# Kernel tuning notes

Measured on AMD Instinct MI355X. Metric: run time of the kernel, lower is better.

The kernel has to match this reference:

```python
import jax, jax.numpy as jnp
import numpy as np

N = 40000   # nodes
E = 600000  # edges
F = 128     # feature/hidden dim
G = 64      # graphs in batch


def setup_inputs() -> dict:
    key = jax.random.key(0)
    ks = jax.random.split(key, 16)
    x = jax.random.normal(ks[0], (N, F), dtype=jnp.float32)
    src = jax.random.randint(ks[1], (E,), 0, N)
    dst = jax.random.randint(ks[2], (E,), 0, N)
    edge_index = jnp.stack([src, dst]).astype(jnp.int64)
    batch = jnp.sort(jax.random.randint(ks[3], (N,), 0, G)).astype(jnp.int64)
    s = 1.0 / np.sqrt(F)
    W0 = jax.random.normal(ks[4], (F, F), dtype=jnp.float32) * s
    b0 = jnp.zeros((F,), dtype=jnp.float32)
    W1 = jax.random.normal(ks[5], (F, F), dtype=jnp.float32) * s
    b1 = jnp.zeros((F,), dtype=jnp.float32)
    W2 = jax.random.normal(ks[6], (F, F), dtype=jnp.float32) * s
    b2 = jnp.zeros((F,), dtype=jnp.float32)
    lin_w = jax.random.normal(ks[7], (F, 1), dtype=jnp.float32) * s
    lin_b = jnp.zeros((1,), dtype=jnp.float32)
    return {"x": x, "edge_index": edge_index, "batch": batch,
            "W0": W0, "b0": b0, "W1": W1, "b1": b1, "W2": W2, "b2": b2,
            "lin_w": lin_w, "lin_b": lin_b}


def _gcn_conv(x, W, b, src, dst, norm, num_nodes):
    # PyG GCNConv: linear transform, gather source, normalize, scatter-add to dst, add bias
    h = x @ W                                  # [N, F_out]
    msg = h[src] * norm[:, None]               # [E+N, F_out]
    agg = jax.ops.segment_sum(msg, dst, num_segments=num_nodes)
    return agg + b


def reference(x, edge_index, batch, W0, b0, W1, b1, W2, b2, lin_w, lin_b):
    num_nodes = x.shape[0]
    loops = jnp.arange(num_nodes, dtype=edge_index.dtype)
    src = jnp.concatenate([edge_index[0], loops])   # add self-loops
    dst = jnp.concatenate([edge_index[1], loops])
    # symmetric normalization deg^-1/2 (degree over in-edges incl. self loops)
    deg = jax.ops.segment_sum(jnp.ones_like(src, dtype=x.dtype), dst,
                              num_segments=num_nodes)
    dinv = jnp.where(deg > 0, jax.lax.rsqrt(jnp.maximum(deg, 1e-12)), 0.0)
    norm = dinv[src] * dinv[dst]                    # [E+N]

    h = jax.nn.relu(_gcn_conv(x, W0, b0, src, dst, norm, num_nodes))
    h = jax.nn.relu(_gcn_conv(h, W1, b1, src, dst, norm, num_nodes))
    h = jax.nn.relu(_gcn_conv(h, W2, b2, src, dst, norm, num_nodes))

    # global_mean_pool over ragged graph segments
    sums = jax.ops.segment_sum(h, batch, num_segments=G)            # [G, F]
    counts = jax.ops.segment_sum(jnp.ones((num_nodes,), h.dtype), batch,
                                 num_segments=G)                    # [G]
    pooled = sums / jnp.maximum(counts, 1.0)[:, None]
    return pooled @ lin_w + lin_b                                   # [G, 1]
```

## Files before the change

### kernel.cpp

```cpp
#include <hip/hip_runtime.h>
#include <hip/hip_bf16.h>

#define F_DIM 128
#define POOL_SEG 16

typedef __attribute__((ext_vector_type(8))) short short8v;
typedef __attribute__((ext_vector_type(4))) float float4v;


__device__ __forceinline__ ushort f2bf(float f) {
    uint u = __float_as_uint(f);
    u += 0x7fffu + ((u >> 16) & 1u);
    return (ushort)(u >> 16);
}
__device__ __forceinline__ float bf2f(ushort h) {
    return __uint_as_float(((uint)h) << 16);
}
__device__ __forceinline__ void bf2x(uint u, float& a, float& b) {
    a = __uint_as_float((u & 0x0000ffffu) << 16);
    b = __uint_as_float(u & 0xffff0000u);
}


__global__ void count_kernel(const int* __restrict__ dst, int* __restrict__ deg, int E_) {
    int i = blockIdx.x * blockDim.x + threadIdx.x;
    if (i < E_) atomicAdd(&deg[dst[i]], 1);
}

__global__ void scan_blocksums_kernel(const int* __restrict__ deg, int* __restrict__ bsum, int N_) {
    __shared__ int s[256];
    int i = blockIdx.x * 256 + threadIdx.x;
    s[threadIdx.x] = (i < N_) ? deg[i] : 0;
    __syncthreads();
    for (int off = 128; off; off >>= 1) {
        if (threadIdx.x < off) s[threadIdx.x] += s[threadIdx.x + off];
        __syncthreads();
    }
    if (threadIdx.x == 0) bsum[blockIdx.x] = s[0];
}

__global__ void scan_bs_kernel(const int* __restrict__ bsum, int* __restrict__ bsx, int NB) {
    __shared__ int s[256];
    int t = threadIdx.x;
    int orig = (t < NB) ? bsum[t] : 0;
    s[t] = orig;
    __syncthreads();
    for (int off = 1; off < 256; off <<= 1) {
        int v = (t >= off) ? s[t - off] : 0;
        __syncthreads();
        s[t] += v;
        __syncthreads();
    }
    if (t < NB) bsx[t] = s[t] - orig;
}

__global__ void scan_final_kernel(const int* __restrict__ deg, const int* __restrict__ bsx,
                                  int* __restrict__ row_ptr, int* __restrict__ rfill,
                                  float* __restrict__ dinv, int N_, int E_) {
    __shared__ int s[256];
    int t = threadIdx.x;
    int i = blockIdx.x * 256 + t;
    int orig = (i < N_) ? deg[i] : 0;
    s[t] = orig;
    __syncthreads();
    for (int off = 1; off < 256; off <<= 1) {
        int v = (t >= off) ? s[t - off] : 0;
        __syncthreads();
        s[t] += v;
        __syncthreads();
    }
    int excl = s[t] - orig + bsx[blockIdx.x];
    if (i < N_) {
        row_ptr[i] = excl;
        rfill[i] = excl;
        dinv[i] = 1.0f / sqrtf((float)(orig + 1));
    }
    if (i == N_ - 1) row_ptr[N_] = E_;
}

__global__ void fill_kernel(const int* __restrict__ src, const int* __restrict__ dst,
                            int* __restrict__ cur, int* __restrict__ col_src, int E_) {
    int i = blockIdx.x * blockDim.x + threadIdx.x;
    if (i < E_) {
        int p = atomicAdd(&cur[dst[i]], 1);
        col_src[p] = src[i];
    }
}


__global__ __launch_bounds__(256) void wprep_kernel(
    const float* __restrict__ W0, const float* __restrict__ W1, const float* __restrict__ W2,
    ushort* __restrict__ Wth, ushort* __restrict__ Wtl)
{
    int layer = blockIdx.x >> 4;
    int chunkc = blockIdx.x & 15;
    const float* W = (layer == 0) ? W0 : (layer == 1) ? W1 : W2;
    int t = threadIdx.x;
    int c  = chunkc * 8 + (t >> 5);
    int k0 = (t & 31) * 4;
    ushort4 hi, lo;
    float v0 = W[(size_t)(k0 + 0) * F_DIM + c];
    float v1 = W[(size_t)(k0 + 1) * F_DIM + c];
    float v2 = W[(size_t)(k0 + 2) * F_DIM + c];
    float v3 = W[(size_t)(k0 + 3) * F_DIM + c];
    hi.x = f2bf(v0); lo.x = f2bf(v0 - bf2f(hi.x));
    hi.y = f2bf(v1); lo.y = f2bf(v1 - bf2f(hi.y));
    hi.z = f2bf(v2); lo.z = f2bf(v2 - bf2f(hi.z));
    hi.w = f2bf(v3); lo.w = f2bf(v3 - bf2f(hi.w));
    size_t o = (size_t)layer * F_DIM * F_DIM + (size_t)c * F_DIM + k0;
    *reinterpret_cast<ushort4*>(&Wth[o]) = hi;
    *reinterpret_cast<ushort4*>(&Wtl[o]) = lo;
}


__global__ __launch_bounds__(256) void gemm_scale_kernel(
    const float* __restrict__ in, const ushort* __restrict__ Wth, const ushort* __restrict__ Wtl,
    const float* __restrict__ dinv, ushort* __restrict__ outbf, int N_)
{
    __shared__ ushort Ah[64 * F_DIM];
    __shared__ ushort Al[64 * F_DIM];
    __shared__ ushort Bh[64 * F_DIM];
    __shared__ ushort Bl[64 * F_DIM];

    const int tid = threadIdx.x;
    const int brow = (blockIdx.x >> 1) * 64;
    const int bcol = (blockIdx.x & 1) * 64;

    #pragma unroll
    for (int i = 0; i < 4; ++i) {
        int chunk = tid + i * 256;
        int r  = chunk >> 4;
        int k0 = (chunk & 15) * 8;
        int row = brow + r;
        float f[8];
        if (row < N_) {
            float4 g0 = *reinterpret_cast<const float4*>(&in[(size_t)row * F_DIM + k0]);
            float4 g1 = *reinterpret_cast<const float4*>(&in[(size_t)row * F_DIM + k0 + 4]);
            f[0] = g0.x; f[1] = g0.y; f[2] = g0.z; f[3] = g0.w;
            f[4] = g1.x; f[5] = g1.y; f[6] = g1.z; f[7] = g1.w;
        } else {
            #pragma unroll
            for (int j = 0; j < 8; ++j) f[j] = 0.f;
        }
        ushort hi[8], lo[8];
        #pragma unroll
        for (int j = 0; j < 8; ++j) {
            hi[j] = f2bf(f[j]);
            lo[j] = f2bf(f[j] - bf2f(hi[j]));
        }
        int idx = r * F_DIM + (k0 ^ ((r & 7) << 3));
        *reinterpret_cast<short8v*>(&Ah[idx]) = *reinterpret_cast<short8v*>(hi);
        *reinterpret_cast<short8v*>(&Al[idx]) = *reinterpret_cast<short8v*>(lo);
    }
    #pragma unroll
    for (int i = 0; i < 4; ++i) {
        int chunk = tid + i * 256;
        int c  = chunk >> 4;
        int k0 = (chunk & 15) * 8;
        size_t go = (size_t)(bcol + c) * F_DIM + k0;
        int idx = c * F_DIM + (k0 ^ ((c & 7) << 3));
        *reinterpret_cast<short8v*>(&Bh[idx]) = *reinterpret_cast<const short8v*>(&Wth[go]);
        *reinterpret_cast<short8v*>(&Bl[idx]) = *reinterpret_cast<const short8v*>(&Wtl[go]);
    }
    __syncthreads();

    const int l = tid & 63;
    const int wave = tid >> 6;
    const int m0 = wave * 16;
    const int row_a = m0 + (l & 15);
    const int kgrp = (l >> 4) * 8;
    const int aswz = (row_a & 7) << 3;

    float4v acc[4] = {{0.f,0.f,0.f,0.f},{0.f,0.f,0.f,0.f},{0.f,0.f,0.f,0.f},{0.f,0.f,0.f,0.f}};

    #pragma unroll
    for (int kk = 0; kk < 4; ++kk) {
        int kbase = kk * 32 + kgrp;
        short8v a_h = *reinterpret_cast<short8v*>(&Ah[row_a * F_DIM + (kbase ^ aswz)]);
        short8v a_l = *reinterpret_cast<short8v*>(&Al[row_a * F_DIM + (kbase ^ aswz)]);
        #pragma unroll
        for (int n = 0; n < 4; ++n) {
            int col_b = n * 16 + (l & 15);
            int bidx = col_b * F_DIM + (kbase ^ ((col_b & 7) << 3));
            short8v b_h = *reinterpret_cast<short8v*>(&Bh[bidx]);
            short8v b_l = *reinterpret_cast<short8v*>(&Bl[bidx]);
            acc[n] = __builtin_amdgcn_mfma_f32_16x16x32_bf16(a_h, b_h, acc[n], 0, 0, 0);
            acc[n] = __builtin_amdgcn_mfma_f32_16x16x32_bf16(a_l, b_h, acc[n], 0, 0, 0);
            acc[n] = __builtin_amdgcn_mfma_f32_16x16x32_bf16(a_h, b_l, acc[n], 0, 0, 0);
        }
    }

    #pragma unroll
    for (int i = 0; i < 4; ++i) {
        int rloc = m0 + (l >> 4) * 4 + i;
        int row = brow + rloc;
        if (row < N_) {
            float s = dinv[row];
            #pragma unroll
            for (int n = 0; n < 4; ++n) {
                ushort o = f2bf(s * acc[n][i]);
                outbf[(size_t)row * F_DIM + bcol + n * 16 + (l & 15)] = o;
            }
        }
    }
}


__global__ __launch_bounds__(256) void gather_kernel(
    const ushort* __restrict__ Mbf, const int* __restrict__ row_ptr,
    const int* __restrict__ col_src, const float* __restrict__ dinv,
    const float* __restrict__ bias, float* __restrict__ Hout, int N_)
{
    int v = blockIdx.x * 4 + (threadIdx.x >> 6);
    if (v >= N_) return;
    const int lane = threadIdx.x & 63;
    const int fq  = lane & 15;
    const int sub = lane >> 4;
    const uint4* M4 = reinterpret_cast<const uint4*>(Mbf);

    float acc[8];
    if (sub == 0) {
        uint4 u = M4[(size_t)v * 16 + fq];
        bf2x(u.x, acc[0], acc[1]);
        bf2x(u.y, acc[2], acc[3]);
        bf2x(u.z, acc[4], acc[5]);
        bf2x(u.w, acc[6], acc[7]);
    } else {
        #pragma unroll
        for (int j = 0; j < 8; ++j) acc[j] = 0.f;
    }

    int lo = row_ptr[v], hi = row_ptr[v + 1];
    int e = lo;
    for (; e + 12 <= hi; e += 12) {
        int s0 = col_src[e + sub];
        int s1 = col_src[e + 4 + sub];
        int s2 = col_src[e + 8 + sub];
        uint4 u0 = M4[(size_t)s0 * 16 + fq];
        uint4 u1 = M4[(size_t)s1 * 16 + fq];
        uint4 u2 = M4[(size_t)s2 * 16 + fq];
        float a, b;
        bf2x(u0.x, a, b); acc[0] += a; acc[1] += b;
        bf2x(u0.y, a, b); acc[2] += a; acc[3] += b;
        bf2x(u0.z, a, b); acc[4] += a; acc[5] += b;
        bf2x(u0.w, a, b); acc[6] += a; acc[7] += b;
        bf2x(u1.x, a, b); acc[0] += a; acc[1] += b;
        bf2x(u1.y, a, b); acc[2] += a; acc[3] += b;
        bf2x(u1.z, a, b); acc[4] += a; acc[5] += b;
        bf2x(u1.w, a, b); acc[6] += a; acc[7] += b;
        bf2x(u2.x, a, b); acc[0] += a; acc[1] += b;
        bf2x(u2.y, a, b); acc[2] += a; acc[3] += b;
        bf2x(u2.z, a, b); acc[4] += a; acc[5] += b;
        bf2x(u2.w, a, b); acc[6] += a; acc[7] += b;
    }
    for (; e + 4 <= hi; e += 4) {
        int s = col_src[e + sub];
        uint4 u = M4[(size_t)s * 16 + fq];
        float a, b;
        bf2x(u.x, a, b); acc[0] += a; acc[1] += b;
        bf2x(u.y, a, b); acc[2] += a; acc[3] += b;
        bf2x(u.z, a, b); acc[4] += a; acc[5] += b;
        bf2x(u.w, a, b); acc[6] += a; acc[7] += b;
    }
    if (e + sub < hi) {
        int s = col_src[e + sub];
        uint4 u = M4[(size_t)s * 16 + fq];
        float a, b;
        bf2x(u.x, a, b); acc[0] += a; acc[1] += b;
        bf2x(u.y, a, b); acc[2] += a; acc[3] += b;
        bf2x(u.z, a, b); acc[4] += a; acc[5] += b;
        bf2x(u.w, a, b); acc[6] += a; acc[7] += b;
    }

    #pragma unroll
    for (int j = 0; j < 8; ++j) {
        acc[j] += __shfl_xor(acc[j], 16);
        acc[j] += __shfl_xor(acc[j], 32);
    }

    if (sub == 0) {
        float dv = dinv[v];
        const float4* b4 = reinterpret_cast<const float4*>(bias);
        float4 bb0 = b4[fq * 2], bb1 = b4[fq * 2 + 1];
        float4 o0, o1;
        o0.x = fmaxf(dv * acc[0] + bb0.x, 0.0f);
        o0.y = fmaxf(dv * acc[1] + bb0.y, 0.0f);
        o0.z = fmaxf(dv * acc[2] + bb0.z, 0.0f);
        o0.w = fmaxf(dv * acc[3] + bb0.w, 0.0f);
        o1.x = fmaxf(dv * acc[4] + bb1.x, 0.0f);
        o1.y = fmaxf(dv * acc[5] + bb1.y, 0.0f);
        o1.z = fmaxf(dv * acc[6] + bb1.z, 0.0f);
        o1.w = fmaxf(dv * acc[7] + bb1.w, 0.0f);
        float4* H4 = reinterpret_cast<float4*>(&Hout[(size_t)v * F_DIM + fq * 8]);
        H4[0] = o0;
        H4[1] = o1;
    }
}


__device__ __forceinline__ int lower_bound_i(const int* __restrict__ a, int n, int key) {
    int lo = 0, hi = n;
    while (lo < hi) {
        int mid = (lo + hi) >> 1;
        if (a[mid] < key) lo = mid + 1; else hi = mid;
    }
    return lo;
}

__global__ __launch_bounds__(128) void pool_part_kernel(
    const float* __restrict__ H, const int* __restrict__ batch,
    float* __restrict__ partial, int N_)
{
    int g = blockIdx.x / POOL_SEG;
    int s = blockIdx.x % POOL_SEG;
    int lo = lower_bound_i(batch, N_, g);
    int hi = lower_bound_i(batch, N_, g + 1);
    int len = hi - lo;
    int chunk = (len + POOL_SEG - 1) / POOL_SEG;
    int a = lo + s * chunk;
    int b = min(a + chunk, hi);
    int col = threadIdx.x;
    float acc = 0.f;
    for (int n = a; n < b; ++n) acc += H[(size_t)n * F_DIM + col];
    partial[((size_t)g * POOL_SEG + s) * F_DIM + col] = acc;
}

__global__ __launch_bounds__(128) void pool_final_kernel(
    const float* __restrict__ partial, const int* __restrict__ batch,
    const float* __restrict__ lin_w, const float* __restrict__ lin_b,
    float* __restrict__ out, int N_)
{
    int g = blockIdx.x;
    int col = threadIdx.x;
    float acc = 0.f;
    #pragma unroll
    for (int s = 0; s < POOL_SEG; ++s)
        acc += partial[((size_t)g * POOL_SEG + s) * F_DIM + col];
    int lo = lower_bound_i(batch, N_, g);
    int hi = lower_bound_i(batch, N_, g + 1);
    float pooled = acc / fmaxf((float)(hi - lo), 1.0f);
    float v = pooled * lin_w[col];
    __shared__ float sm[128];
    sm[col] = v;
    __syncthreads();
    if (col < 64) {
        float t = sm[col] + sm[col + 64];
        for (int off = 32; off; off >>= 1) t += __shfl_down(t, off);
        if (col == 0) out[g] = t + lin_b[0];
    }
}


extern "C" void kernel_launch(void* const* d_in, const int* in_sizes, int n_in,
                              void* d_out, int out_size, void* d_ws, size_t ws_size,
                              hipStream_t stream) {
    const float* x     = (const float*)d_in[0];
    const int*   ei    = (const int*)d_in[1];
    const int*   batch = (const int*)d_in[2];
    const float* W0    = (const float*)d_in[3];
    const float* b0    = (const float*)d_in[4];
    const float* W1    = (const float*)d_in[5];
    const float* b1    = (const float*)d_in[6];
    const float* W2    = (const float*)d_in[7];
    const float* b2    = (const float*)d_in[8];
    const float* lin_w = (const float*)d_in[9];
    const float* lin_b = (const float*)d_in[10];

    const int N_ = in_sizes[2];
    const int E_ = in_sizes[1] / 2;
    const int G_ = out_size;
    const int* esrc = ei;
    const int* edst = ei + E_;

    char* p = reinterpret_cast<char*>(d_ws);
    ushort* Mbf = reinterpret_cast<ushort*>(p);        p += (size_t)N_ * F_DIM * sizeof(ushort);
    float*  Hbuf = reinterpret_cast<float*>(p);        p += (size_t)N_ * F_DIM * sizeof(float);
    float*  dinvp = reinterpret_cast<float*>(p);       p += (size_t)N_ * sizeof(float);
    int*    deg = reinterpret_cast<int*>(p);           p += (size_t)N_ * sizeof(int);
    int*    row_ptr = reinterpret_cast<int*>(p);       p += (size_t)(N_ + 4) * sizeof(int);
    int*    rfill = reinterpret_cast<int*>(p);         p += (size_t)N_ * sizeof(int);
    int*    col_src = reinterpret_cast<int*>(p);       p += (size_t)E_ * sizeof(int);
    ushort* Wth = reinterpret_cast<ushort*>(p);        p += (size_t)3 * F_DIM * F_DIM * sizeof(ushort);
    ushort* Wtl = reinterpret_cast<ushort*>(p);        p += (size_t)3 * F_DIM * F_DIM * sizeof(ushort);
    const int NB = (N_ + 255) / 256;
    int*    bsum = reinterpret_cast<int*>(p);          p += (size_t)NB * sizeof(int);
    int*    bsx = reinterpret_cast<int*>(p);
    float*  partial = reinterpret_cast<float*>(d_ws);

    hipMemsetAsync(deg, 0, (size_t)N_ * sizeof(int), stream);

    int eb = (E_ + 255) / 256;
    wprep_kernel<<<48, 256, 0, stream>>>(W0, W1, W2, Wth, Wtl);
    count_kernel<<<eb, 256, 0, stream>>>(edst, deg, E_);
    scan_blocksums_kernel<<<NB, 256, 0, stream>>>(deg, bsum, N_);
    scan_bs_kernel<<<1, 256, 0, stream>>>(bsum, bsx, NB);
    scan_final_kernel<<<NB, 256, 0, stream>>>(deg, bsx, row_ptr, rfill, dinvp, N_, E_);
    fill_kernel<<<eb, 256, 0, stream>>>(esrc, edst, rfill, col_src, E_);

    const int gemm_grid = ((N_ + 63) / 64) * 2;
    const int gat_grid  = (N_ + 3) / 4;

    const float* cur_in = x;
    const float* bias[3] = {b0, b1, b2};
    for (int l = 0; l < 3; ++l) {
        gemm_scale_kernel<<<gemm_grid, 256, 0, stream>>>(
            cur_in, Wth + (size_t)l * F_DIM * F_DIM, Wtl + (size_t)l * F_DIM * F_DIM,
            dinvp, Mbf, N_);
        gather_kernel<<<gat_grid, 256, 0, stream>>>(
            Mbf, row_ptr, col_src, dinvp, bias[l], Hbuf, N_);
        cur_in = Hbuf;
    }

    pool_part_kernel<<<G_ * POOL_SEG, 128, 0, stream>>>(Hbuf, batch, partial, N_);
    pool_final_kernel<<<G_, 128, 0, stream>>>(partial, batch, lin_w, lin_b, (float*)d_out, N_);
}
```

Measured before the change: 228.2 us.

## Cooperatively load neighbor indices per wave and fold deg zeroing into prep kernel

The gather kernel now loads up to 64 neighbor indices at once, one per lane, with the self-loop treated as the first entry. Lanes then broadcast indices with shuffles and issue four row loads per iteration, and a masked tail handles the remainder. This replaces per-subgroup scalar col_src loads and the separate self-row load, aiming for more memory-level parallelism and fewer dependent index loads. Separately, the hipMemsetAsync on deg is replaced by extra blocks in the weight-prep kernel, which removes one launch. The masked tail may fetch redundant rows for low-degree nodes.

New measurement: 214.1 us, median of 2. -6.2%, faster.

```diff
diff --git a/kernel.cpp b/kernel.cpp
--- a/kernel.cpp
+++ b/kernel.cpp
@@ -88,10 +88,15 @@
 }
 
 
-__global__ __launch_bounds__(256) void wprep_kernel(
+__global__ __launch_bounds__(256) void prep_kernel(
     const float* __restrict__ W0, const float* __restrict__ W1, const float* __restrict__ W2,
-    ushort* __restrict__ Wth, ushort* __restrict__ Wtl)
+    ushort* __restrict__ Wth, ushort* __restrict__ Wtl, int* __restrict__ deg, int N_)
 {
+    if (blockIdx.x >= 48) {
+        int i = (blockIdx.x - 48) * 256 + threadIdx.x;
+        if (i < N_) deg[i] = 0;
+        return;
+    }
     int layer = blockIdx.x >> 4;
     int chunkc = blockIdx.x & 15;
     const float* W = (layer == 0) ? W0 : (layer == 1) ? W1 : W2;
@@ -219,57 +224,84 @@
     const uint4* M4 = reinterpret_cast<const uint4*>(Mbf);
 
     float acc[8];
-    if (sub == 0) {
-        uint4 u = M4[(size_t)v * 16 + fq];
-        bf2x(u.x, acc[0], acc[1]);
-        bf2x(u.y, acc[2], acc[3]);
-        bf2x(u.z, acc[4], acc[5]);
-        bf2x(u.w, acc[6], acc[7]);
-    } else {
-        #pragma unroll
-        for (int j = 0; j < 8; ++j) acc[j] = 0.f;
-    }
-
-    int lo = row_ptr[v], hi = row_ptr[v + 1];
-    int e = lo;
-    for (; e + 12 <= hi; e += 12) {
-        int s0 = col_src[e + sub];
-        int s1 = col_src[e + 4 + sub];
-        int s2 = col_src[e + 8 + sub];
-        uint4 u0 = M4[(size_t)s0 * 16 + fq];
-        uint4 u1 = M4[(size_t)s1 * 16 + fq];
-        uint4 u2 = M4[(size_t)s2 * 16 + fq];
-        float a, b;
-        bf2x(u0.x, a, b); acc[0] += a; acc[1] += b;
-        bf2x(u0.y, a, b); acc[2] += a; acc[3] += b;
-        bf2x(u0.z, a, b); acc[4] += a; acc[5] += b;
-        bf2x(u0.w, a, b); acc[6] += a; acc[7] += b;
-        bf2x(u1.x, a, b); acc[0] += a; acc[1] += b;
-        bf2x(u1.y, a, b); acc[2] += a; acc[3] += b;
-        bf2x(u1.z, a, b); acc[4] += a; acc[5] += b;
-        bf2x(u1.w, a, b); acc[6] += a; acc[7] += b;
-        bf2x(u2.x, a, b); acc[0] += a; acc[1] += b;
-        bf2x(u2.y, a, b); acc[2] += a; acc[3] += b;
-        bf2x(u2.z, a, b); acc[4] += a; acc[5] += b;
-        bf2x(u2.w, a, b); acc[6] += a; acc[7] += b;
-    }
-    for (; e + 4 <= hi; e += 4) {
-        int s = col_src[e + sub];
-        uint4 u = M4[(size_t)s * 16 + fq];
-        float a, b;
-        bf2x(u.x, a, b); acc[0] += a; acc[1] += b;
-        bf2x(u.y, a, b); acc[2] += a; acc[3] += b;
-        bf2x(u.z, a, b); acc[4] += a; acc[5] += b;
-        bf2x(u.w, a, b); acc[6] += a; acc[7] += b;
-    }
-    if (e + sub < hi) {
-        int s = col_src[e + sub];
-        uint4 u = M4[(size_t)s * 16 + fq];
-        float a, b;
-        bf2x(u.x, a, b); acc[0] += a; acc[1] += b;
-        bf2x(u.y, a, b); acc[2] += a; acc[3] += b;
-        bf2x(u.z, a, b); acc[4] += a; acc[5] += b;
-        bf2x(u.w, a, b); acc[6] += a; acc[7] += b;
+    #pragma unroll
+    for (int j = 0; j < 8; ++j) acc[j] = 0.f;
+
+    int lo = row_ptr[v];
+    int total = row_ptr[v + 1] - lo + 1;
+
+    for (int base = 0; base < total; base += 64) {
+        int nidx = total - base; if (nidx > 64) nidx = 64;
+        int p = base + lane;
+        int idx = v;
+        if (p > 0 && p < total) idx = col_src[lo + p - 1];
+
+        int nslots = (nidx + 3) >> 2;
+        int jfull  = (nidx >> 4) * 4;
+        int j = 0;
+        for (; j < jfull; j += 4) {
+            int q0 = j * 4 + sub;
+            int s0 = __shfl(idx, q0);
+            int s1 = __shfl(idx, q0 + 4);
+            int s2 = __shfl(idx, q0 + 8);
+            int s3 = __shfl(idx, q0 + 12);
+            uint4 u0 = M4[(size_t)s0 * 16 + fq];
+            uint4 u1 = M4[(size_t)s1 * 16 + fq];
+            uint4 u2 = M4[(size_t)s2 * 16 + fq];
+            uint4 u3 = M4[(size_t)s3 * 16 + fq];
+            float a, b;
+            bf2x(u0.x, a, b); acc[0] += a; acc[1] += b;
+            bf2x(u0.y, a, b); acc[2] += a; acc[3] += b;
+            bf2x(u0.z, a, b); acc[4] += a; acc[5] += b;
+            bf2x(u0.w, a, b); acc[6] += a; acc[7] += b;
+            bf2x(u1.x, a, b); acc[0] += a; acc[1] += b;
+            bf2x(u1.y, a, b); acc[2] += a; acc[3] += b;
+            bf2x(u1.z, a, b); acc[4] += a; acc[5] += b;
+            bf2x(u1.w, a, b); acc[6] += a; acc[7] += b;
+            bf2x(u2.x, a, b); acc[0] += a; acc[1] += b;
+            bf2x(u2.y, a, b); acc[2] += a; acc[3] += b;
+            bf2x(u2.z, a, b); acc[4] += a; acc[5] += b;
+            bf2x(u2.w, a, b); acc[6] += a; acc[7] += b;
+            bf2x(u3.x, a, b); acc[0] += a; acc[1] += b;
+            bf2x(u3.y, a, b); acc[2] += a; acc[3] += b;
+            bf2x(u3.z, a, b); acc[4] += a; acc[5] += b;
+            bf2x(u3.w, a, b); acc[6] += a; acc[7] += b;
+        }
+        if (j < nslots) {
+            int q0 = j * 4 + sub;
+            int q1 = q0 + 4, q2 = q0 + 8, q3 = q0 + 12;
+            int c0 = min(q0, nidx - 1), c1 = min(q1, nidx - 1);
+            int c2 = min(q2, nidx - 1), c3 = min(q3, nidx - 1);
+            int s0 = __shfl(idx, c0);
+            int s1 = __shfl(idx, c1);
+            int s2 = __shfl(idx, c2);
+            int s3 = __shfl(idx, c3);
+            float m0 = (q0 < nidx) ? 1.f : 0.f;
+            float m1 = (q1 < nidx) ? 1.f : 0.f;
+            float m2 = (q2 < nidx) ? 1.f : 0.f;
+            float m3 = (q3 < nidx) ? 1.f : 0.f;
+            uint4 u0 = M4[(size_t)s0 * 16 + fq];
+            uint4 u1 = M4[(size_t)s1 * 16 + fq];
+            uint4 u2 = M4[(size_t)s2 * 16 + fq];
+            uint4 u3 = M4[(size_t)s3 * 16 + fq];
+            float a, b;
+            bf2x(u0.x, a, b); acc[0] = fmaf(a, m0, acc[0]); acc[1] = fmaf(b, m0, acc[1]);
+            bf2x(u0.y, a, b); acc[2] = fmaf(a, m0, acc[2]); acc[3] = fmaf(b, m0, acc[3]);
+            bf2x(u0.z, a, b); acc[4] = fmaf(a, m0, acc[4]); acc[5] = fmaf(b, m0, acc[5]);
+            bf2x(u0.w, a, b); acc[6] = fmaf(a, m0, acc[6]); acc[7] = fmaf(b, m0, acc[7]);
+            bf2x(u1.x, a, b); acc[0] = fmaf(a, m1, acc[0]); acc[1] = fmaf(b, m1, acc[1]);
+            bf2x(u1.y, a, b); acc[2] = fmaf(a, m1, acc[2]); acc[3] = fmaf(b, m1, acc[3]);
+            bf2x(u1.z, a, b); acc[4] = fmaf(a, m1, acc[4]); acc[5] = fmaf(b, m1, acc[5]);
+            bf2x(u1.w, a, b); acc[6] = fmaf(a, m1, acc[6]); acc[7] = fmaf(b, m1, acc[7]);
+            bf2x(u2.x, a, b); acc[0] = fmaf(a, m2, acc[0]); acc[1] = fmaf(b, m2, acc[1]);
+            bf2x(u2.y, a, b); acc[2] = fmaf(a, m2, acc[2]); acc[3] = fmaf(b, m2, acc[3]);
+            bf2x(u2.z, a, b); acc[4] = fmaf(a, m2, acc[4]); acc[5] = fmaf(b, m2, acc[5]);
+            bf2x(u2.w, a, b); acc[6] = fmaf(a, m2, acc[6]); acc[7] = fmaf(b, m2, acc[7]);
+            bf2x(u3.x, a, b); acc[0] = fmaf(a, m3, acc[0]); acc[1] = fmaf(b, m3, acc[1]);
+            bf2x(u3.y, a, b); acc[2] = fmaf(a, m3, acc[2]); acc[3] = fmaf(b, m3, acc[3]);
+            bf2x(u3.z, a, b); acc[4] = fmaf(a, m3, acc[4]); acc[5] = fmaf(b, m3, acc[5]);
+            bf2x(u3.w, a, b); acc[6] = fmaf(a, m3, acc[6]); acc[7] = fmaf(b, m3, acc[7]);
+        }
     }
 
     #pragma unroll
@@ -387,10 +419,8 @@
     int*    bsx = reinterpret_cast<int*>(p);
     float*  partial = reinterpret_cast<float*>(d_ws);
 
-    hipMemsetAsync(deg, 0, (size_t)N_ * sizeof(int), stream);
-
     int eb = (E_ + 255) / 256;
-    wprep_kernel<<<48, 256, 0, stream>>>(W0, W1, W2, Wth, Wtl);
+    prep_kernel<<<48 + NB, 256, 0, stream>>>(W0, W1, W2, Wth, Wtl, deg, N_);
     count_kernel<<<eb, 256, 0, stream>>>(edst, deg, E_);
     scan_blocksums_kernel<<<NB, 256, 0, stream>>>(deg, bsum, N_);
     scan_bs_kernel<<<1, 256, 0, stream>>>(bsum, bsx, NB);
```
